# Kernel tuning notes

Hardware: AMD Instinct MI355X
Metric: run time of the kernel (lower is better)

## Reference

```python
import jax, jax.numpy as jnp
import numpy as np

D_MODEL = 1024
N_HEADS = 16
D_K = D_MODEL // N_HEADS
D_FF = 4096
EPS = 1e-5


def layer_norm(x, g, b):
    mu = jnp.mean(x, axis=-1, keepdims=True)
    var = jnp.var(x, axis=-1, keepdims=True)
    return (x - mu) * jax.lax.rsqrt(var + EPS) * g + b


def setup_inputs() -> dict:
    key = jax.random.key(0)
    ks = jax.random.split(key, 16)
    B, S = 4, 2048
    s_in = 1.0 / np.sqrt(D_MODEL)
    s_ff = 1.0 / np.sqrt(D_FF)
    return {
        "x": jax.random.normal(ks[0], (B, S, D_MODEL), jnp.float32),
        "mask": jnp.ones((B, 1, 1, S), jnp.int32),
        "Wq": jax.random.normal(ks[1], (D_MODEL, D_MODEL), jnp.float32) * s_in,
        "bq": jnp.zeros((D_MODEL,), jnp.float32),
        "Wk": jax.random.normal(ks[2], (D_MODEL, D_MODEL), jnp.float32) * s_in,
        "bk": jnp.zeros((D_MODEL,), jnp.float32),
        "Wv": jax.random.normal(ks[3], (D_MODEL, D_MODEL), jnp.float32) * s_in,
        "bv": jnp.zeros((D_MODEL,), jnp.float32),
        "Wo": jax.random.normal(ks[4], (D_MODEL, D_MODEL), jnp.float32) * s_in,
        "bo": jnp.zeros((D_MODEL,), jnp.float32),
        "W1": jax.random.normal(ks[5], (D_MODEL, D_FF), jnp.float32) * s_in,
        "b1": jnp.zeros((D_FF,), jnp.float32),
        "W2": jax.random.normal(ks[6], (D_FF, D_MODEL), jnp.float32) * s_ff,
        "b2": jnp.zeros((D_MODEL,), jnp.float32),
        "ln1_g": jnp.ones((D_MODEL,), jnp.float32),
        "ln1_b": jnp.zeros((D_MODEL,), jnp.float32),
        "ln2_g": jnp.ones((D_MODEL,), jnp.float32),
        "ln2_b": jnp.zeros((D_MODEL,), jnp.float32),
    }


def reference(x, mask, Wq, bq, Wk, bk, Wv, bv, Wo, bo, W1, b1, W2, b2,
              ln1_g, ln1_b, ln2_g, ln2_b):
    B, S, _ = x.shape
    h = layer_norm(x, ln1_g, ln1_b)  # norm1(x), used for q/k/v
    # project and split heads: [B,S,D] -> [B,H,S,Dk]
    def heads(t):
        return t.reshape(B, S, N_HEADS, D_K).transpose(0, 2, 1, 3)
    Q = heads(h @ Wq + bq)
    K = heads(h @ Wk + bk)
    V = heads(h @ Wv + bv)
    scores = jnp.einsum('bhqd,bhkd->bhqk', Q, K) / jnp.sqrt(jnp.float32(D_K))
    scores = jnp.where(mask == 0, jnp.float32(-1e9), scores)
    attn = jax.nn.softmax(scores, axis=-1)
    out = jnp.einsum('bhqk,bhkd->bhqd', attn, V)
    out = out.transpose(0, 2, 1, 3).reshape(B, S, D_MODEL)
    attn_out = out @ Wo + bo
    x = x + attn_out
    # FFN with pre-norm (torch nn.GELU default = exact erf gelu)
    h2 = layer_norm(x, ln2_g, ln2_b)
    ff = jax.nn.gelu(h2 @ W1 + b1, approximate=False) @ W2 + b2
    return x + ff
```

## Files before the change

### kernel.cpp

```cpp
#include <hip/hip_runtime.h>
#include <stdint.h>
#include <string.h>


typedef unsigned int       u32;
typedef unsigned short     u16;
typedef __bf16 bf16x8 __attribute__((ext_vector_type(8)));
typedef float  floatx4 __attribute__((ext_vector_type(4)));

#define D_MODEL 1024
#define N_HEADS 16
#define D_K     64
#define D_FF    4096
#define S_LEN   2048
#define N_TOK   8192
#define LDQKV   3072

__device__ __forceinline__ u16 f2b(float f) {
    u32 u = __float_as_uint(f);
    u32 r = (u + 0x7fffu + ((u >> 16) & 1u)) >> 16;
    return (u16)r;
}

__device__ __forceinline__ float fast_gelu(float x) {
    float t = x * x;
    float y = x * 1.5957691216057308f * fmaf(t, 0.044715f, 1.0f);
    return x * __builtin_amdgcn_rcpf(1.0f + __expf(-y));
}

__device__ __forceinline__ void gl_lds16(const void* g, void* l) {
    __builtin_amdgcn_global_load_lds(
        (const __attribute__((address_space(1))) u32*)g,
        (__attribute__((address_space(3))) u32*)l, 16, 0, 0);
}

__global__ __launch_bounds__(256) void transpose_bf16_kernel(
    const float* __restrict__ src, u16* __restrict__ dst, int R, int C)
{
    __shared__ float tile[32][33];
    int cb = blockIdx.x * 32, rb = blockIdx.y * 32;
    int tx = threadIdx.x & 31, ty = threadIdx.x >> 5;
    #pragma unroll
    for (int yy = ty; yy < 32; yy += 8)
        tile[yy][tx] = src[(size_t)(rb + yy) * C + cb + tx];
    __syncthreads();
    #pragma unroll
    for (int yy = ty; yy < 32; yy += 8)
        dst[(size_t)(cb + yy) * R + rb + tx] = f2b(tile[tx][yy]);
}

__global__ __launch_bounds__(256) void vt_kernel(
    const u16* __restrict__ Qkv, u16* __restrict__ Vt)
{
    __shared__ u32 tile[64 * 65];
    int b = blockIdx.z, h = blockIdx.y, s0 = blockIdx.x * 64;
    int t = threadIdx.x;
    int r = t >> 2, cg = (t & 3) * 16;
    const u16* src = &Qkv[((size_t)(b * S_LEN + s0 + r)) * LDQKV + 2048 + h * D_K + cg];
    uint4 a0 = *(const uint4*)src;
    uint4 a1 = *(const uint4*)(src + 8);
    u16 vals[16];
    memcpy(vals, &a0, 16); memcpy(vals + 8, &a1, 16);
    #pragma unroll
    for (int j = 0; j < 16; j++) tile[r * 65 + cg + j] = vals[j];
    __syncthreads();
    int f = t & 63, w = t >> 6;
    u16 outv[16];
    #pragma unroll
    for (int j = 0; j < 16; j++) outv[j] = (u16)tile[(w * 16 + j) * 65 + f];
    uint4 o0, o1; memcpy(&o0, outv, 16); memcpy(&o1, outv + 8, 16);
    u16* dst = &Vt[((size_t)((b * N_HEADS + h) * D_K + f)) * S_LEN + s0 + w * 16];
    *(uint4*)dst = o0; *(uint4*)(dst + 8) = o1;
}

__global__ __launch_bounds__(256) void ln_kernel(
    const float* __restrict__ x, const float* __restrict__ g,
    const float* __restrict__ b, u16* __restrict__ out)
{
    int row = blockIdx.x;
    int t = threadIdx.x;
    const float4* xr = reinterpret_cast<const float4*>(x + (size_t)row * D_MODEL);
    float4 v = xr[t];
    float s  = v.x + v.y + v.z + v.w;
    float ss = v.x * v.x + v.y * v.y + v.z * v.z + v.w * v.w;
    #pragma unroll
    for (int off = 32; off >= 1; off >>= 1) {
        s  += __shfl_down(s,  off);
        ss += __shfl_down(ss, off);
    }
    __shared__ float red[8];
    int wid = t >> 6, ln = t & 63;
    if (ln == 0) { red[wid] = s; red[4 + wid] = ss; }
    __syncthreads();
    float S  = red[0] + red[1] + red[2] + red[3];
    float SS = red[4] + red[5] + red[6] + red[7];
    float mu  = S * (1.0f / D_MODEL);
    float var = SS * (1.0f / D_MODEL) - mu * mu;
    float rs  = rsqrtf(var + 1e-5f);
    const float4* g4 = reinterpret_cast<const float4*>(g);
    const float4* b4 = reinterpret_cast<const float4*>(b);
    float4 gv = g4[t], bv = b4[t];
    float y0 = (v.x - mu) * rs * gv.x + bv.x;
    float y1 = (v.y - mu) * rs * gv.y + bv.y;
    float y2 = (v.z - mu) * rs * gv.z + bv.z;
    float y3 = (v.w - mu) * rs * gv.w + bv.w;
    uint2 pk;
    pk.x = (u32)f2b(y0) | ((u32)f2b(y1) << 16);
    pk.y = (u32)f2b(y2) | ((u32)f2b(y3) << 16);
    *reinterpret_cast<uint2*>(out + (size_t)row * D_MODEL + t * 4) = pk;
}

__global__ __launch_bounds__(256) void gemm_bt(
    const u16* __restrict__ A, const u16* __restrict__ Bt,
    const float* __restrict__ bias, const float* __restrict__ biasK,
    const float* __restrict__ biasV, const float* __restrict__ resid,
    float* __restrict__ outF, u16* __restrict__ outB,
    int M, int N, int K, int flags)
{
    __shared__ u16 As[128 * 32];
    __shared__ u16 Bs[128 * 32];

    int nbx = N >> 7, nby = M >> 7;
    int bid = blockIdx.x;
    int xcd = bid & 7, p = bid >> 3;
    int bandsz = nby >> 3;
    int m0 = (xcd * bandsz + p / nbx) * 128;
    int n0 = (p % nbx) * 128;

    int t = threadIdx.x;
    int wave = t >> 6, lane = t & 63, quad = lane >> 4, lr = lane & 15;
    int wm = (wave >> 1) * 64, wn = (wave & 1) * 64;

    floatx4 acc[4][4] = {};

    int s0 = t,       r0 = s0 >> 2, g0 = ((s0 & 3) ^ ((r0 >> 1) & 3)) * 8;
    int s1 = t + 256, r1 = s1 >> 2, g1 = ((s1 & 3) ^ ((r1 >> 1) & 3)) * 8;
    int csw = (quad ^ ((lr >> 1) & 3)) * 8;

    for (int k0 = 0; k0 < K; k0 += 32) {
        gl_lds16(&A [(size_t)(m0 + r0) * K + k0 + g0], &As[s0 * 8]);
        gl_lds16(&A [(size_t)(m0 + r1) * K + k0 + g1], &As[s1 * 8]);
        gl_lds16(&Bt[(size_t)(n0 + r0) * K + k0 + g0], &Bs[s0 * 8]);
        gl_lds16(&Bt[(size_t)(n0 + r1) * K + k0 + g1], &Bs[s1 * 8]);
        __syncthreads();

        bf16x8 af[4], bfr[4];
        #pragma unroll
        for (int mt = 0; mt < 4; mt++)
            af[mt] = *reinterpret_cast<const bf16x8*>(&As[(wm + mt * 16 + lr) * 32 + csw]);
        #pragma unroll
        for (int nt = 0; nt < 4; nt++)
            bfr[nt] = *reinterpret_cast<const bf16x8*>(&Bs[(wn + nt * 16 + lr) * 32 + csw]);
        #pragma unroll
        for (int mt = 0; mt < 4; mt++)
            #pragma unroll
            for (int nt = 0; nt < 4; nt++)
                acc[mt][nt] = __builtin_amdgcn_mfma_f32_16x16x32_bf16(
                    af[mt], bfr[nt], acc[mt][nt], 0, 0, 0);
        __syncthreads();
    }

    bool do_gelu = (flags & 1) != 0;
    #pragma unroll
    for (int mt = 0; mt < 4; mt++) {
        #pragma unroll
        for (int nt = 0; nt < 4; nt++) {
            int c = n0 + wn + nt * 16 + lr;
            float bsv;
            if (biasK) {
                if (c >= 2048)      bsv = biasV[c - 2048];
                else if (c >= 1024) bsv = biasK[c - 1024];
                else                bsv = bias[c];
            } else {
                bsv = bias[c];
            }
            #pragma unroll
            for (int i = 0; i < 4; i++) {
                int r = m0 + wm + mt * 16 + quad * 4 + i;
                float v = acc[mt][nt][i] + bsv;
                if (resid) v += resid[(size_t)r * N + c];
                if (do_gelu) v = fast_gelu(v);
                if (outF) outF[(size_t)r * N + c] = v;
                if (outB) outB[(size_t)r * N + c] = f2b(v);
            }
        }
    }
}

__global__ __launch_bounds__(256, 4) void attn_mfma_kernel(
    const u16* __restrict__ Qkv, const u16* __restrict__ Vt,
    const int* __restrict__ mask, u16* __restrict__ ctx)
{
    __shared__ u16 Ks[64 * 72];
    __shared__ u16 Vs[64 * 72];
    __shared__ u16 Ps[128 * 72];
    __shared__ float Ms[64];

    int b = blockIdx.z, h = blockIdx.y;
    int q0 = blockIdx.x * 128;
    int t = threadIdx.x;
    int wave = t >> 6, lane = t & 63, quad = lane >> 4, lr = lane & 15;
    int wm = wave * 32;

    bf16x8 qf[2][2];
    #pragma unroll
    for (int mt = 0; mt < 2; mt++)
        #pragma unroll
        for (int kk = 0; kk < 2; kk++)
            qf[mt][kk] = *(const bf16x8*)&Qkv[((size_t)(b * S_LEN + q0 + wm + mt * 16 + lr)) * LDQKV
                                              + h * D_K + kk * 32 + quad * 8];

    floatx4 o[2][4] = {};
    float lsum[2][4] = {};
    const float scale = 0.125f;

    for (int kt = 0; kt < S_LEN / 64; kt++) {
        __syncthreads();
        {
            int row = t >> 2, cg = (t & 3) * 16;
            const u16* kg = &Qkv[((size_t)(b * S_LEN + kt * 64 + row)) * LDQKV + 1024 + h * D_K + cg];
            *(uint4*)&Ks[row * 72 + cg]     = *(const uint4*)kg;
            *(uint4*)&Ks[row * 72 + cg + 8] = *(const uint4*)(kg + 8);
            const u16* vg = &Vt[((size_t)((b * N_HEADS + h) * D_K + row)) * S_LEN + kt * 64 + cg];
            *(uint4*)&Vs[row * 72 + cg]     = *(const uint4*)vg;
            *(uint4*)&Vs[row * 72 + cg + 8] = *(const uint4*)(vg + 8);
            if (t < 64) Ms[t] = (mask[b * S_LEN + kt * 64 + t] == 0) ? -1e9f : 0.0f;
        }
        __syncthreads();

        floatx4 s[2][4] = {};
        #pragma unroll
        for (int kk = 0; kk < 2; kk++) {
            bf16x8 bk[4];
            #pragma unroll
            for (int n = 0; n < 4; n++)
                bk[n] = *(const bf16x8*)&Ks[(n * 16 + lr) * 72 + kk * 32 + quad * 8];
            #pragma unroll
            for (int mt = 0; mt < 2; mt++)
                #pragma unroll
                for (int n = 0; n < 4; n++)
                    s[mt][n] = __builtin_amdgcn_mfma_f32_16x16x32_bf16(
                        qf[mt][kk], bk[n], s[mt][n], 0, 0, 0);
        }

        #pragma unroll
        for (int mt = 0; mt < 2; mt++) {
            #pragma unroll
            for (int n = 0; n < 4; n++) {
                float msk = Ms[n * 16 + lr];
                #pragma unroll
                for (int i = 0; i < 4; i++) {
                    float p = __expf(s[mt][n][i] * scale + msk);
                    lsum[mt][i] += p;
                    Ps[(wm + mt * 16 + quad * 4 + i) * 72 + n * 16 + lr] = f2b(p);
                }
            }
        }

        bf16x8 bv[4][2];
        #pragma unroll
        for (int kk = 0; kk < 2; kk++)
            #pragma unroll
            for (int n = 0; n < 4; n++)
                bv[n][kk] = *(const bf16x8*)&Vs[(n * 16 + lr) * 72 + kk * 32 + quad * 8];

        __syncthreads();

        #pragma unroll
        for (int kk = 0; kk < 2; kk++) {
            #pragma unroll
            for (int mt = 0; mt < 2; mt++) {
                bf16x8 ap = *(const bf16x8*)&Ps[(wm + mt * 16 + lr) * 72 + kk * 32 + quad * 8];
                #pragma unroll
                for (int n = 0; n < 4; n++)
                    o[mt][n] = __builtin_amdgcn_mfma_f32_16x16x32_bf16(
                        ap, bv[n][kk], o[mt][n], 0, 0, 0);
            }
        }
    }

    #pragma unroll
    for (int mt = 0; mt < 2; mt++)
        #pragma unroll
        for (int i = 0; i < 4; i++) {
            float v = lsum[mt][i];
            v += __shfl_xor(v, 1);
            v += __shfl_xor(v, 2);
            v += __shfl_xor(v, 4);
            v += __shfl_xor(v, 8);
            lsum[mt][i] = 1.0f / v;
        }
    #pragma unroll
    for (int mt = 0; mt < 2; mt++)
        #pragma unroll
        for (int n = 0; n < 4; n++)
            #pragma unroll
            for (int i = 0; i < 4; i++) {
                int row = q0 + wm + mt * 16 + quad * 4 + i;
                int col = h * D_K + n * 16 + lr;
                ctx[((size_t)(b * S_LEN + row)) * D_MODEL + col] =
                    f2b(o[mt][n][i] * lsum[mt][i]);
            }
}

extern "C" void kernel_launch(void* const* d_in, const int* in_sizes, int n_in,
                              void* d_out, int out_size, void* d_ws, size_t ws_size,
                              hipStream_t stream)
{
    const float* x    = (const float*)d_in[0];
    const int*   mask = (const int*)  d_in[1];
    const float* Wq   = (const float*)d_in[2];
    const float* bq   = (const float*)d_in[3];
    const float* Wk   = (const float*)d_in[4];
    const float* bk   = (const float*)d_in[5];
    const float* Wv   = (const float*)d_in[6];
    const float* bv   = (const float*)d_in[7];
    const float* Wo   = (const float*)d_in[8];
    const float* bo   = (const float*)d_in[9];
    const float* W1   = (const float*)d_in[10];
    const float* b1   = (const float*)d_in[11];
    const float* W2   = (const float*)d_in[12];
    const float* b2   = (const float*)d_in[13];
    const float* ln1g = (const float*)d_in[14];
    const float* ln1b = (const float*)d_in[15];
    const float* ln2g = (const float*)d_in[16];
    const float* ln2b = (const float*)d_in[17];
    float* out = (float*)d_out;

    char* ws = (char*)d_ws;
    const size_t MB = 1u << 20;
    u16*   wqkvT = (u16*)(ws + 0 * MB);
    u16*   woT   = (u16*)(ws + 6 * MB);
    u16*   w1T   = (u16*)(ws + 8 * MB);
    u16*   w2T   = (u16*)(ws + 16 * MB);
    u16*   h     = (u16*)(ws + 24 * MB);
    u16*   Qkv   = (u16*)(ws + 40 * MB);
    u16*   ctx   = (u16*)(ws + 88 * MB);
    float* x1    = (float*)(ws + 104 * MB);
    u16*   Vt    = h;

    bool full = ws_size >= 216 * MB;
    u16* h2  = full ? (u16*)(ws + 136 * MB) : Qkv;
    u16* ff1 = full ? (u16*)(ws + 152 * MB) : (u16*)(ws + 56 * MB);
    int nchunk = full ? 1 : 2;
    int Mc = N_TOK / nchunk;

    dim3 blk(256);

    transpose_bf16_kernel<<<dim3(32, 32),  blk, 0, stream>>>(Wq, wqkvT,             1024, 1024);
    transpose_bf16_kernel<<<dim3(32, 32),  blk, 0, stream>>>(Wk, wqkvT + 1024*1024, 1024, 1024);
    transpose_bf16_kernel<<<dim3(32, 32),  blk, 0, stream>>>(Wv, wqkvT + 2048*1024, 1024, 1024);
    transpose_bf16_kernel<<<dim3(32, 32),  blk, 0, stream>>>(Wo, woT, 1024, 1024);
    transpose_bf16_kernel<<<dim3(128, 32), blk, 0, stream>>>(W1, w1T, 1024, 4096);
    transpose_bf16_kernel<<<dim3(32, 128), blk, 0, stream>>>(W2, w2T, 4096, 1024);

    ln_kernel<<<N_TOK, blk, 0, stream>>>(x, ln1g, ln1b, h);

    gemm_bt<<<dim3(24 * 64), blk, 0, stream>>>(h, wqkvT, bq, bk, bv, nullptr,
                                               nullptr, Qkv, N_TOK, LDQKV, D_MODEL, 0);

    vt_kernel<<<dim3(32, 16, 4), blk, 0, stream>>>(Qkv, Vt);

    attn_mfma_kernel<<<dim3(16, 16, 4), blk, 0, stream>>>(Qkv, Vt, mask, ctx);

    gemm_bt<<<dim3(8 * 64), blk, 0, stream>>>(ctx, woT, bo, nullptr, nullptr, x,
                                              x1, nullptr, N_TOK, D_MODEL, D_MODEL, 0);

    ln_kernel<<<N_TOK, blk, 0, stream>>>(x1, ln2g, ln2b, h2);

    for (int c = 0; c < nchunk; c++) {
        size_t ro = (size_t)c * Mc * D_MODEL;
        size_t rf = (size_t)c * Mc * D_FF;
        gemm_bt<<<dim3(32 * (Mc / 128)), blk, 0, stream>>>(
            h2 + ro, w1T, b1, nullptr, nullptr, nullptr,
            nullptr, ff1 + (full ? rf : 0), Mc, D_FF, D_MODEL, 1);
        gemm_bt<<<dim3(8 * (Mc / 128)), blk, 0, stream>>>(
            ff1 + (full ? rf : 0), w2T, b2, nullptr, nullptr, x1 + ro,
            out + ro, nullptr, Mc, D_MODEL, D_FF, 0);
    }
}
```

Baseline: 655.7 us.

## Deepen GEMM K-step to 64 and use 64-row tiles for N=1024 GEMMs

The bf16 GEMM is templated on its M tile size. Each K iteration now loads 64 columns instead of 32, using an 8-way XOR swizzle, which halves the number of barrier pairs per output tile. The Wo and W2 projections (N=1024) switch to 64x128 tiles, launching twice as many blocks so the GPU's compute units are better filled. The trade-offs are more shared memory per block, which can lower occupancy, and less operand reuse on the smaller tiles.

```diff
diff --git a/kernel.cpp b/kernel.cpp
--- a/kernel.cpp
+++ b/kernel.cpp
@@ -110,6 +110,7 @@
     *reinterpret_cast<uint2*>(out + (size_t)row * D_MODEL + t * 4) = pk;
 }
 
+template<int MT>
 __global__ __launch_bounds__(256) void gemm_bt(
     const u16* __restrict__ A, const u16* __restrict__ Bt,
     const float* __restrict__ bias, const float* __restrict__ biasK,
@@ -117,52 +118,66 @@
     float* __restrict__ outF, u16* __restrict__ outB,
     int M, int N, int K, int flags)
 {
-    __shared__ u16 As[128 * 32];
-    __shared__ u16 Bs[128 * 32];
-
-    int nbx = N >> 7, nby = M >> 7;
+    constexpr int ATILES = MT / 32;
+    __shared__ u16 As[MT * 64];
+    __shared__ u16 Bs[128 * 64];
+
+    int nbx = N >> 7, nby = M / MT;
     int bid = blockIdx.x;
     int xcd = bid & 7, p = bid >> 3;
     int bandsz = nby >> 3;
-    int m0 = (xcd * bandsz + p / nbx) * 128;
+    int m0 = (xcd * bandsz + p / nbx) * MT;
     int n0 = (p % nbx) * 128;
 
     int t = threadIdx.x;
     int wave = t >> 6, lane = t & 63, quad = lane >> 4, lr = lane & 15;
-    int wm = (wave >> 1) * 64, wn = (wave & 1) * 64;
-
-    floatx4 acc[4][4] = {};
-
-    int s0 = t,       r0 = s0 >> 2, g0 = ((s0 & 3) ^ ((r0 >> 1) & 3)) * 8;
-    int s1 = t + 256, r1 = s1 >> 2, g1 = ((s1 & 3) ^ ((r1 >> 1) & 3)) * 8;
-    int csw = (quad ^ ((lr >> 1) & 3)) * 8;
-
-    for (int k0 = 0; k0 < K; k0 += 32) {
-        gl_lds16(&A [(size_t)(m0 + r0) * K + k0 + g0], &As[s0 * 8]);
-        gl_lds16(&A [(size_t)(m0 + r1) * K + k0 + g1], &As[s1 * 8]);
-        gl_lds16(&Bt[(size_t)(n0 + r0) * K + k0 + g0], &Bs[s0 * 8]);
-        gl_lds16(&Bt[(size_t)(n0 + r1) * K + k0 + g1], &Bs[s1 * 8]);
-        __syncthreads();
-
-        bf16x8 af[4], bfr[4];
-        #pragma unroll
-        for (int mt = 0; mt < 4; mt++)
-            af[mt] = *reinterpret_cast<const bf16x8*>(&As[(wm + mt * 16 + lr) * 32 + csw]);
-        #pragma unroll
-        for (int nt = 0; nt < 4; nt++)
-            bfr[nt] = *reinterpret_cast<const bf16x8*>(&Bs[(wn + nt * 16 + lr) * 32 + csw]);
-        #pragma unroll
-        for (int mt = 0; mt < 4; mt++)
-            #pragma unroll
-            for (int nt = 0; nt < 4; nt++)
-                acc[mt][nt] = __builtin_amdgcn_mfma_f32_16x16x32_bf16(
-                    af[mt], bfr[nt], acc[mt][nt], 0, 0, 0);
+    int wm = (wave >> 1) * (MT / 2), wn = (wave & 1) * 64;
+
+    floatx4 acc[ATILES][4] = {};
+
+    for (int k0 = 0; k0 < K; k0 += 64) {
+        #pragma unroll
+        for (int i = 0; i < MT / 32; i++) {
+            int s = t + i * 256;
+            int row = s >> 3, g = ((s & 7) ^ (row & 7)) * 8;
+            gl_lds16(&A[(size_t)(m0 + row) * K + k0 + g], &As[s * 8]);
+        }
+        #pragma unroll
+        for (int i = 0; i < 4; i++) {
+            int s = t + i * 256;
+            int row = s >> 3, g = ((s & 7) ^ (row & 7)) * 8;
+            gl_lds16(&Bt[(size_t)(n0 + row) * K + k0 + g], &Bs[s * 8]);
+        }
+        __syncthreads();
+
+        #pragma unroll
+        for (int kk = 0; kk < 2; kk++) {
+            bf16x8 af[ATILES], bfr[4];
+            #pragma unroll
+            for (int mt = 0; mt < ATILES; mt++) {
+                int row = wm + mt * 16 + lr;
+                int pg = ((kk * 4 + quad) ^ (row & 7)) * 8;
+                af[mt] = *reinterpret_cast<const bf16x8*>(&As[row * 64 + pg]);
+            }
+            #pragma unroll
+            for (int nt = 0; nt < 4; nt++) {
+                int row = wn + nt * 16 + lr;
+                int pg = ((kk * 4 + quad) ^ (row & 7)) * 8;
+                bfr[nt] = *reinterpret_cast<const bf16x8*>(&Bs[row * 64 + pg]);
+            }
+            #pragma unroll
+            for (int mt = 0; mt < ATILES; mt++)
+                #pragma unroll
+                for (int nt = 0; nt < 4; nt++)
+                    acc[mt][nt] = __builtin_amdgcn_mfma_f32_16x16x32_bf16(
+                        af[mt], bfr[nt], acc[mt][nt], 0, 0, 0);
+        }
         __syncthreads();
     }
 
     bool do_gelu = (flags & 1) != 0;
     #pragma unroll
-    for (int mt = 0; mt < 4; mt++) {
+    for (int mt = 0; mt < ATILES; mt++) {
         #pragma unroll
         for (int nt = 0; nt < 4; nt++) {
             int c = n0 + wn + nt * 16 + lr;
@@ -356,25 +371,25 @@
 
     ln_kernel<<<N_TOK, blk, 0, stream>>>(x, ln1g, ln1b, h);
 
-    gemm_bt<<<dim3(24 * 64), blk, 0, stream>>>(h, wqkvT, bq, bk, bv, nullptr,
-                                               nullptr, Qkv, N_TOK, LDQKV, D_MODEL, 0);
+    gemm_bt<128><<<dim3(24 * 64), blk, 0, stream>>>(h, wqkvT, bq, bk, bv, nullptr,
+                                                    nullptr, Qkv, N_TOK, LDQKV, D_MODEL, 0);
 
     vt_kernel<<<dim3(32, 16, 4), blk, 0, stream>>>(Qkv, Vt);
 
     attn_mfma_kernel<<<dim3(16, 16, 4), blk, 0, stream>>>(Qkv, Vt, mask, ctx);
 
-    gemm_bt<<<dim3(8 * 64), blk, 0, stream>>>(ctx, woT, bo, nullptr, nullptr, x,
-                                              x1, nullptr, N_TOK, D_MODEL, D_MODEL, 0);
+    gemm_bt<64><<<dim3(8 * 128), blk, 0, stream>>>(ctx, woT, bo, nullptr, nullptr, x,
+                                                   x1, nullptr, N_TOK, D_MODEL, D_MODEL, 0);
 
     ln_kernel<<<N_TOK, blk, 0, stream>>>(x1, ln2g, ln2b, h2);
 
     for (int c = 0; c < nchunk; c++) {
         size_t ro = (size_t)c * Mc * D_MODEL;
         size_t rf = (size_t)c * Mc * D_FF;
-        gemm_bt<<<dim3(32 * (Mc / 128)), blk, 0, stream>>>(
+        gemm_bt<128><<<dim3(32 * (Mc / 128)), blk, 0, stream>>>(
             h2 + ro, w1T, b1, nullptr, nullptr, nullptr,
             nullptr, ff1 + (full ? rf : 0), Mc, D_FF, D_MODEL, 1);
-        gemm_bt<<<dim3(8 * (Mc / 128)), blk, 0, stream>>>(
+        gemm_bt<64><<<dim3(8 * (Mc / 64)), blk, 0, stream>>>(
             ff1 + (full ? rf : 0), w2T, b2, nullptr, nullptr, x1 + ro,
             out + ro, nullptr, Mc, D_MODEL, D_FF, 0);
     }
```

Result: faster. 616.8 us (-5.9%).
